# Optimization experiments

Hardware: AMD Instinct MI355X
Metric: run time of the kernel (lower is better)

The kernel has to match this reference:

```python
import jax, jax.numpy as jnp
import numpy as np

B, S, D, H = 2, 2048, 1024, 16
DH = D // H  # dim_per_head = 64


def setup_inputs() -> dict:
    key = jax.random.key(0)
    ks = jax.random.split(key, 12)
    scale = 1.0 / np.sqrt(D)
    inp = {
        "key": jax.random.normal(ks[0], (B, S, D), jnp.float32),
        "value": jax.random.normal(ks[1], (B, S, D), jnp.float32),
        "query": jax.random.normal(ks[2], (B, S, D), jnp.float32),
        "mask": jax.random.randint(ks[3], (B, S, S), 0, 2) == 1,
        "Wq": jax.random.normal(ks[4], (D, D), jnp.float32) * scale,
        "bq": jnp.zeros((D,), jnp.float32),
        "Wk": jax.random.normal(ks[5], (D, D), jnp.float32) * scale,
        "bk": jnp.zeros((D,), jnp.float32),
        "Wv": jax.random.normal(ks[6], (D, D), jnp.float32) * scale,
        "bv": jnp.zeros((D,), jnp.float32),
        "Wo": jax.random.normal(ks[7], (D, D), jnp.float32) * scale,
        "bo": jnp.zeros((D,), jnp.float32),
    }
    return inp


def reference(key, value, query, mask, Wq, bq, Wk, bk, Wv, bv, Wo, bo):
    b, s, d = query.shape
    dh = d // H

    def split_heads(x):  # [b, s, d] -> [b, H, s, dh]
        return x.reshape(b, -1, H, dh).transpose(0, 2, 1, 3)

    q = split_heads(query @ Wq + bq) / jnp.sqrt(jnp.float32(dh))
    k = split_heads(key @ Wk + bk)
    v = split_heads(value @ Wv + bv)

    scores = jnp.einsum("bhqd,bhkd->bhqk", q, k)  # [b, H, s, s]
    scores = jnp.where(mask[:, None, :, :], jnp.float32(-1e18), scores)
    attn = jax.nn.softmax(scores, axis=-1)  # dropout is identity in eval
    ctx = jnp.einsum("bhqk,bhkd->bhqd", attn, v)
    ctx = ctx.transpose(0, 2, 1, 3).reshape(b, s, d)
    return ctx @ Wo + bo
```

## Files before the change

kernel.cpp:

```cpp
#include <hip/hip_runtime.h>
#include <hip/hip_bf16.h>

#define BATCH  2
#define SEQ    2048
#define DMODEL 1024
#define NHEAD  16
#define DHEAD  64
#define NTOK   (BATCH * SEQ)

using f32x4 = __attribute__((ext_vector_type(4))) float;
using s16x4 = __attribute__((ext_vector_type(4))) short;
using s16x8 = __attribute__((ext_vector_type(8))) short;

__device__ __forceinline__ short f2bf(float f) {
  __hip_bfloat16 h = __float2bfloat16(f);
  return *(short*)&h;
}

__device__ __forceinline__ void gload_lds16(const short* g, short* l) {
  __builtin_amdgcn_global_load_lds(
      (const __attribute__((address_space(1))) void*)g,
      (__attribute__((address_space(3))) void*)l, 16, 0, 0);
}

__global__ __launch_bounds__(256) void wtrans_kernel(
    const float* __restrict__ Wq, const float* __restrict__ Wk,
    const float* __restrict__ Wv, const float* __restrict__ Wo,
    short* __restrict__ Wt) {
  __shared__ short tile[64][72];
  const float* W = blockIdx.z == 0 ? Wq : blockIdx.z == 1 ? Wk
                 : blockIdx.z == 2 ? Wv : Wo;
  short* out = Wt + (size_t)blockIdx.z * DMODEL * DMODEL;
  int k0 = blockIdx.x * 64, n0 = blockIdx.y * 64;
  int t = threadIdx.x;
#pragma unroll
  for (int i = 0; i < 4; ++i) {
    int idx = t + i * 256;
    int row = idx >> 4, c4 = idx & 15;
    f32x4 v = *(const f32x4*)(W + (size_t)(k0 + row) * DMODEL + n0 + c4 * 4);
    s16x4 p;
    p[0] = f2bf(v[0]); p[1] = f2bf(v[1]); p[2] = f2bf(v[2]); p[3] = f2bf(v[3]);
    *(s16x4*)&tile[row][c4 * 4] = p;
  }
  __syncthreads();
#pragma unroll
  for (int i = 0; i < 2; ++i) {
    int idx = t + i * 256;
    int nrow = idx >> 3, c8 = idx & 7;
    s16x8 p;
#pragma unroll
    for (int j = 0; j < 8; ++j) p[j] = tile[c8 * 8 + j][nrow];
    *(s16x8*)(out + (size_t)(n0 + nrow) * DMODEL + k0 + c8 * 8) = p;
  }
}

__global__ __launch_bounds__(256) void mpack_kernel(
    const int* __restrict__ mask, unsigned long long* __restrict__ Mp) {
  const int total_words = BATCH * SEQ * (SEQ / 64);
  int lane = threadIdx.x & 63;
  int wv = blockIdx.x * 4 + (threadIdx.x >> 6);
  int nw = gridDim.x * 4;
  for (int w = wv; w < total_words; w += nw) {
    int mv = mask[(size_t)w * 64 + lane];
    unsigned long long bits = __ballot(mv != 0);
    if (lane == 0) Mp[w] = bits;
  }
}

__global__ __launch_bounds__(256) void proj_qkv_kernel(
    const float* __restrict__ Xq, const float* __restrict__ Xk,
    const float* __restrict__ Xv, const short* __restrict__ Wt,
    const float* __restrict__ bq, const float* __restrict__ bk,
    const float* __restrict__ bv, short* __restrict__ QKV) {
  __shared__ short As[128][32];
  __shared__ short Bs[128][32];
  const int sel = blockIdx.z;
  const float* X    = sel == 0 ? Xq : sel == 1 ? Xk : Xv;
  const float* bias = sel == 0 ? bq : sel == 1 ? bk : bv;
  const short* Wsel = Wt + (size_t)sel * DMODEL * DMODEL;
  short* Obuf = QKV + (size_t)sel * ((size_t)BATCH * NHEAD * SEQ * DHEAD);
  const float scale = sel == 0 ? 0.18033688011111793f : 1.0f;

  int m0 = blockIdx.x * 128, n0 = blockIdx.y * 128;
  int t = threadIdx.x, wid = t >> 6, lane = t & 63;
  int lr = lane & 15, lg = lane >> 4;
  int wr = wid >> 1, wc = wid & 1;
  f32x4 acc[4][4] = {};

  for (int kt = 0; kt < DMODEL / 32; ++kt) {
    int k0 = kt * 32;
    __syncthreads();
#pragma unroll
    for (int i = 0; i < 2; ++i) {
      int c = i * 256 + t;
      short* lbase = &Bs[0][0] + (size_t)((i * 256 + (t & ~63)) << 3);
      gload_lds16(Wsel + (size_t)(n0 + (c >> 2)) * DMODEL + k0 + ((c & 3) << 3),
                  lbase);
    }
#pragma unroll
    for (int i = 0; i < 2; ++i) {
      int idx = t + i * 256, row = idx >> 2, c8 = idx & 3;
      const float* src = X + (size_t)(m0 + row) * DMODEL + k0 + c8 * 8;
      f32x4 v0 = *(const f32x4*)src;
      f32x4 v1 = *(const f32x4*)(src + 4);
      s16x8 p;
      p[0] = f2bf(v0[0]); p[1] = f2bf(v0[1]); p[2] = f2bf(v0[2]); p[3] = f2bf(v0[3]);
      p[4] = f2bf(v1[0]); p[5] = f2bf(v1[1]); p[6] = f2bf(v1[2]); p[7] = f2bf(v1[3]);
      *(s16x8*)&As[row][c8 * 8] = p;
    }
    __syncthreads();
    s16x8 afr[4], bfr[4];
#pragma unroll
    for (int mi = 0; mi < 4; ++mi)
      afr[mi] = *(const s16x8*)&As[wr * 64 + mi * 16 + lr][lg * 8];
#pragma unroll
    for (int ni = 0; ni < 4; ++ni)
      bfr[ni] = *(const s16x8*)&Bs[wc * 64 + ni * 16 + lr][lg * 8];
#pragma unroll
    for (int mi = 0; mi < 4; ++mi)
#pragma unroll
      for (int ni = 0; ni < 4; ++ni)
        acc[mi][ni] = __builtin_amdgcn_mfma_f32_16x16x32_bf16(
            afr[mi], bfr[ni], acc[mi][ni], 0, 0, 0);
  }
#pragma unroll
  for (int mi = 0; mi < 4; ++mi)
#pragma unroll
    for (int ni = 0; ni < 4; ++ni) {
      int n = n0 + wc * 64 + ni * 16 + lr;
      float bv_ = bias[n];
      int h = n >> 6, d = n & 63;
#pragma unroll
      for (int r = 0; r < 4; ++r) {
        int m = m0 + wr * 64 + mi * 16 + lg * 4 + r;
        int b = m >> 11, s = m & (SEQ - 1);
        float val = (acc[mi][ni][r] + bv_) * scale;
        Obuf[((size_t)(b * NHEAD + h) * SEQ + s) * DHEAD + d] = f2bf(val);
      }
    }
}

__global__ __launch_bounds__(256) void attn_kernel(
    const short* __restrict__ Qb, const short* __restrict__ Kb,
    const short* __restrict__ Vb, const unsigned long long* __restrict__ Mp,
    short* __restrict__ Ctx) {
  __shared__ short Ks[64][72];
  __shared__ short Vt[64][72];
  __shared__ short Ps[4][16][72];
  int qt = blockIdx.x, bh = blockIdx.y;
  int b = bh >> 4, h = bh & 15;
  int q0 = qt * 64;
  int t = threadIdx.x, wid = t >> 6, lane = t & 63;
  int lr = lane & 15, lg = lane >> 4;

  const short* Qrow = Qb + ((size_t)bh * SEQ + q0 + wid * 16 + lr) * DHEAD;
  s16x8 qf[2];
  qf[0] = *(const s16x8*)(Qrow + lg * 8);
  qf[1] = *(const s16x8*)(Qrow + 32 + lg * 8);

  float m_run = -1e30f, l_run = 0.f;
  f32x4 o_acc[4] = {};

  const unsigned long long* mrow =
      Mp + ((size_t)b * SEQ + q0 + wid * 16 + lr) * (SEQ / 64);

  for (int kt = 0; kt < SEQ / 64; ++kt) {
    int k0 = kt * 64;
    unsigned long long mw = mrow[kt];
    __syncthreads();
#pragma unroll
    for (int i = 0; i < 2; ++i) {
      int idx = t + i * 256, key = idx >> 3, c8 = idx & 7;
      *(s16x8*)&Ks[key][c8 * 8] =
          *(const s16x8*)(Kb + ((size_t)bh * SEQ + k0 + key) * DHEAD + c8 * 8);
    }
#pragma unroll
    for (int i = 0; i < 2; ++i) {
      int idx = t + i * 256, key = idx & 63, c8 = idx >> 6;
      s16x8 v = *(const s16x8*)(Vb + ((size_t)bh * SEQ + k0 + key) * DHEAD + c8 * 8);
#pragma unroll
      for (int j = 0; j < 8; ++j) Vt[c8 * 8 + j][key] = v[j];
    }
    __syncthreads();

    f32x4 sfr[4];
#pragma unroll
    for (int nf = 0; nf < 4; ++nf) {
      s16x8 kf0 = *(const s16x8*)&Ks[nf * 16 + lr][lg * 8];
      s16x8 kf1 = *(const s16x8*)&Ks[nf * 16 + lr][32 + lg * 8];
      f32x4 c = {};
      c = __builtin_amdgcn_mfma_f32_16x16x32_bf16(kf0, qf[0], c, 0, 0, 0);
      c = __builtin_amdgcn_mfma_f32_16x16x32_bf16(kf1, qf[1], c, 0, 0, 0);
      sfr[nf] = c;
    }
    unsigned w0 = (unsigned)(mw >> (lg * 4));
    unsigned w1 = (unsigned)(mw >> (lg * 4 + 32));
#pragma unroll
    for (int nf = 0; nf < 4; ++nf)
#pragma unroll
      for (int r = 0; r < 4; ++r) {
        unsigned bit = (nf < 2) ? (w0 >> (nf * 16 + r)) : (w1 >> ((nf - 2) * 16 + r));
        if (bit & 1u) sfr[nf][r] = -1e30f;
      }
    float tm = fmaxf(fmaxf(fmaxf(sfr[0][0], sfr[0][1]), fmaxf(sfr[0][2], sfr[0][3])),
                     fmaxf(fmaxf(sfr[1][0], sfr[1][1]), fmaxf(sfr[1][2], sfr[1][3])));
    float tm2 = fmaxf(fmaxf(fmaxf(sfr[2][0], sfr[2][1]), fmaxf(sfr[2][2], sfr[2][3])),
                      fmaxf(fmaxf(sfr[3][0], sfr[3][1]), fmaxf(sfr[3][2], sfr[3][3])));
    tm = fmaxf(tm, tm2);
    tm = fmaxf(tm, __shfl_xor(tm, 16, 64));
    tm = fmaxf(tm, __shfl_xor(tm, 32, 64));

    bool small = __all(tm <= m_run + 8.0f);
    if (!small) {
      float mnew = fmaxf(m_run, tm);
      float scl = __builtin_amdgcn_exp2f(m_run - mnew);
      m_run = mnew;
      l_run *= scl;
      float scl_o[4];
#pragma unroll
      for (int r = 0; r < 4; ++r) scl_o[r] = __shfl(scl, lg * 4 + r, 64);
#pragma unroll
      for (int nf = 0; nf < 4; ++nf)
#pragma unroll
        for (int r = 0; r < 4; ++r) o_acc[nf][r] *= scl_o[r];
    }
    float ps4[4];
#pragma unroll
    for (int nf = 0; nf < 4; ++nf) {
#pragma unroll
      for (int r = 0; r < 4; ++r)
        sfr[nf][r] = __builtin_amdgcn_exp2f(sfr[nf][r] - m_run);
      ps4[nf] = (sfr[nf][0] + sfr[nf][1]) + (sfr[nf][2] + sfr[nf][3]);
    }
    float ps = (ps4[0] + ps4[1]) + (ps4[2] + ps4[3]);
    ps += __shfl_xor(ps, 16, 64);
    ps += __shfl_xor(ps, 32, 64);
    l_run += ps;

#pragma unroll
    for (int nf = 0; nf < 4; ++nf) {
      s16x4 pk;
#pragma unroll
      for (int r = 0; r < 4; ++r) pk[r] = f2bf(sfr[nf][r]);
      *(s16x4*)&Ps[wid][lr][nf * 16 + lg * 4] = pk;
    }
    asm volatile("s_waitcnt lgkmcnt(0)" ::: "memory");
    __builtin_amdgcn_sched_barrier(0);

#pragma unroll
    for (int ks = 0; ks < 2; ++ks) {
      s16x8 pf = *(const s16x8*)&Ps[wid][lr][ks * 32 + lg * 8];
#pragma unroll
      for (int nf = 0; nf < 4; ++nf) {
        s16x8 vf = *(const s16x8*)&Vt[nf * 16 + lr][ks * 32 + lg * 8];
        o_acc[nf] = __builtin_amdgcn_mfma_f32_16x16x32_bf16(pf, vf, o_acc[nf], 0, 0, 0);
      }
    }
  }
  float l_o[4];
#pragma unroll
  for (int r = 0; r < 4; ++r) l_o[r] = __shfl(l_run, lg * 4 + r, 64);
#pragma unroll
  for (int nf = 0; nf < 4; ++nf)
#pragma unroll
    for (int r = 0; r < 4; ++r) {
      int srow = q0 + wid * 16 + lg * 4 + r;
      float val = o_acc[nf][r] / l_o[r];
      Ctx[((size_t)b * SEQ + srow) * DMODEL + h * DHEAD + nf * 16 + lr] = f2bf(val);
    }
}

__global__ __launch_bounds__(256) void proj_out_kernel(
    const short* __restrict__ Ctx, const short* __restrict__ Wot,
    const float* __restrict__ bo, float* __restrict__ Out) {
  __shared__ short As[128][32];
  __shared__ short Bs[128][32];
  int m0 = blockIdx.x * 128, n0 = blockIdx.y * 128;
  int t = threadIdx.x, wid = t >> 6, lane = t & 63;
  int lr = lane & 15, lg = lane >> 4;
  int wr = wid >> 1, wc = wid & 1;
  f32x4 acc[4][4] = {};

  for (int kt = 0; kt < DMODEL / 32; ++kt) {
    int k0 = kt * 32;
    __syncthreads();
#pragma unroll
    for (int i = 0; i < 2; ++i) {
      int c = i * 256 + t;
      size_t lofs = (size_t)((i * 256 + (t & ~63)) << 3);
      gload_lds16(Ctx + (size_t)(m0 + (c >> 2)) * DMODEL + k0 + ((c & 3) << 3),
                  &As[0][0] + lofs);
      gload_lds16(Wot + (size_t)(n0 + (c >> 2)) * DMODEL + k0 + ((c & 3) << 3),
                  &Bs[0][0] + lofs);
    }
    __syncthreads();
    s16x8 afr[4], bfr[4];
#pragma unroll
    for (int mi = 0; mi < 4; ++mi)
      afr[mi] = *(const s16x8*)&As[wr * 64 + mi * 16 + lr][lg * 8];
#pragma unroll
    for (int ni = 0; ni < 4; ++ni)
      bfr[ni] = *(const s16x8*)&Bs[wc * 64 + ni * 16 + lr][lg * 8];
#pragma unroll
    for (int mi = 0; mi < 4; ++mi)
#pragma unroll
      for (int ni = 0; ni < 4; ++ni)
        acc[mi][ni] = __builtin_amdgcn_mfma_f32_16x16x32_bf16(
            afr[mi], bfr[ni], acc[mi][ni], 0, 0, 0);
  }
#pragma unroll
  for (int mi = 0; mi < 4; ++mi)
#pragma unroll
    for (int ni = 0; ni < 4; ++ni) {
      int n = n0 + wc * 64 + ni * 16 + lr;
      float bv_ = bo[n];
#pragma unroll
      for (int r = 0; r < 4; ++r) {
        int m = m0 + wr * 64 + mi * 16 + lg * 4 + r;
        Out[(size_t)m * DMODEL + n] = acc[mi][ni][r] + bv_;
      }
    }
}

extern "C" void kernel_launch(void* const* d_in, const int* in_sizes, int n_in,
                              void* d_out, int out_size, void* d_ws, size_t ws_size,
                              hipStream_t stream) {
  const float* key_in   = (const float*)d_in[0];
  const float* value_in = (const float*)d_in[1];
  const float* query_in = (const float*)d_in[2];
  const int*   mask     = (const int*)d_in[3];
  const float* Wq = (const float*)d_in[4];
  const float* bq = (const float*)d_in[5];
  const float* Wk = (const float*)d_in[6];
  const float* bk = (const float*)d_in[7];
  const float* Wv = (const float*)d_in[8];
  const float* bv = (const float*)d_in[9];
  const float* Wo = (const float*)d_in[10];
  const float* bo = (const float*)d_in[11];
  float* out = (float*)d_out;

  short* ws = (short*)d_ws;
  const size_t WSZ   = (size_t)DMODEL * DMODEL;
  const size_t QKVSZ = (size_t)BATCH * NHEAD * SEQ * DHEAD;
  short* Wt  = ws;
  short* QKV = ws + 4 * WSZ;
  short* Qb  = QKV;
  short* Kb  = QKV + QKVSZ;
  short* Vb  = QKV + 2 * QKVSZ;
  short* Ctx = QKV + 3 * QKVSZ;
  unsigned long long* Mp = (unsigned long long*)ws;

  wtrans_kernel<<<dim3(16, 16, 4), 256, 0, stream>>>(Wq, Wk, Wv, Wo, Wt);
  proj_qkv_kernel<<<dim3(32, 8, 3), 256, 0, stream>>>(
      query_in, key_in, value_in, Wt, bq, bk, bv, QKV);
  mpack_kernel<<<dim3(1024), 256, 0, stream>>>(mask, Mp);
  attn_kernel<<<dim3(32, 32), 256, 0, stream>>>(Qb, Kb, Vb, Mp, Ctx);
  proj_out_kernel<<<dim3(32, 8), 256, 0, stream>>>(Ctx, Wt + 3 * WSZ, bo, out);
}
```

Baseline: 194.9 us.

## Prefetch next K/V tile into registers, XOR-swizzle LDS, and raise MFMA priority

The attention kernel now loads the next K/V tile and mask word into registers while the current tile is being computed, which hides global-load latency behind the MFMA work. The padded LDS arrays are replaced by unpadded ones with an XOR swizzle on 8-element chunks, so K, V-transpose and P accesses avoid bank conflicts with less shared memory. s_setprio is raised around the MFMA sections. The cost is extra registers for the prefetch buffers, which may reduce occupancy.

```diff
diff --git a/kernel.cpp b/kernel.cpp
--- a/kernel.cpp
+++ b/kernel.cpp
@@ -144,57 +144,79 @@
     const short* __restrict__ Qb, const short* __restrict__ Kb,
     const short* __restrict__ Vb, const unsigned long long* __restrict__ Mp,
     short* __restrict__ Ctx) {
-  __shared__ short Ks[64][72];
-  __shared__ short Vt[64][72];
-  __shared__ short Ps[4][16][72];
+  __shared__ short Ks[64 * 64];
+  __shared__ short Vt[64 * 64];
+  __shared__ short Ps[4 * 16 * 64];
   int qt = blockIdx.x, bh = blockIdx.y;
   int b = bh >> 4, h = bh & 15;
   int q0 = qt * 64;
   int t = threadIdx.x, wid = t >> 6, lane = t & 63;
   int lr = lane & 15, lg = lane >> 4;
+  int lr7 = lr & 7;
 
   const short* Qrow = Qb + ((size_t)bh * SEQ + q0 + wid * 16 + lr) * DHEAD;
   s16x8 qf[2];
   qf[0] = *(const s16x8*)(Qrow + lg * 8);
   qf[1] = *(const s16x8*)(Qrow + 32 + lg * 8);
 
+  const short* KbBase = Kb + (size_t)bh * SEQ * DHEAD;
+  const short* VbBase = Vb + (size_t)bh * SEQ * DHEAD;
+
   float m_run = -1e30f, l_run = 0.f;
   f32x4 o_acc[4] = {};
 
   const unsigned long long* mrow =
       Mp + ((size_t)b * SEQ + q0 + wid * 16 + lr) * (SEQ / 64);
+  unsigned long long mw = mrow[0];
+
+  s16x8 kreg[2], vreg[2];
+#pragma unroll
+  for (int i = 0; i < 2; ++i) {
+    kreg[i] = *(const s16x8*)(KbBase + (size_t)((t >> 3) + i * 32) * DHEAD + (t & 7) * 8);
+    vreg[i] = *(const s16x8*)(VbBase + (size_t)lane * DHEAD + (wid + i * 4) * 8);
+  }
 
   for (int kt = 0; kt < SEQ / 64; ++kt) {
-    int k0 = kt * 64;
-    unsigned long long mw = mrow[kt];
+    unsigned long long mw_cur = mw;
     __syncthreads();
 #pragma unroll
     for (int i = 0; i < 2; ++i) {
-      int idx = t + i * 256, key = idx >> 3, c8 = idx & 7;
-      *(s16x8*)&Ks[key][c8 * 8] =
-          *(const s16x8*)(Kb + ((size_t)bh * SEQ + k0 + key) * DHEAD + c8 * 8);
-    }
-#pragma unroll
-    for (int i = 0; i < 2; ++i) {
-      int idx = t + i * 256, key = idx & 63, c8 = idx >> 6;
-      s16x8 v = *(const s16x8*)(Vb + ((size_t)bh * SEQ + k0 + key) * DHEAD + c8 * 8);
-#pragma unroll
-      for (int j = 0; j < 8; ++j) Vt[c8 * 8 + j][key] = v[j];
-    }
-    __syncthreads();
+      int krow = (t >> 3) + i * 32, kc = t & 7;
+      *(s16x8*)&Ks[krow * 64 + ((kc ^ (krow & 7)) << 3)] = kreg[i];
+      int vc8 = wid + i * 4;
+#pragma unroll
+      for (int j = 0; j < 8; ++j) {
+        int d = vc8 * 8 + j;
+        Vt[d * 64 + ((((lane >> 3) ^ (d & 7)) << 3) | (lane & 7))] = vreg[i][j];
+      }
+    }
+    __syncthreads();
+    if (kt + 1 < SEQ / 64) {
+      int k0n = (kt + 1) * 64;
+#pragma unroll
+      for (int i = 0; i < 2; ++i) {
+        kreg[i] = *(const s16x8*)(KbBase + (size_t)(k0n + (t >> 3) + i * 32) * DHEAD + (t & 7) * 8);
+        vreg[i] = *(const s16x8*)(VbBase + (size_t)(k0n + lane) * DHEAD + (wid + i * 4) * 8);
+      }
+      mw = mrow[kt + 1];
+    }
 
     f32x4 sfr[4];
+    __builtin_amdgcn_s_setprio(1);
 #pragma unroll
     for (int nf = 0; nf < 4; ++nf) {
-      s16x8 kf0 = *(const s16x8*)&Ks[nf * 16 + lr][lg * 8];
-      s16x8 kf1 = *(const s16x8*)&Ks[nf * 16 + lr][32 + lg * 8];
+      int row = nf * 16 + lr;
+      s16x8 kf0 = *(const s16x8*)&Ks[row * 64 + ((lg ^ lr7) << 3)];
+      s16x8 kf1 = *(const s16x8*)&Ks[row * 64 + (((4 + lg) ^ lr7) << 3)];
       f32x4 c = {};
       c = __builtin_amdgcn_mfma_f32_16x16x32_bf16(kf0, qf[0], c, 0, 0, 0);
       c = __builtin_amdgcn_mfma_f32_16x16x32_bf16(kf1, qf[1], c, 0, 0, 0);
       sfr[nf] = c;
     }
-    unsigned w0 = (unsigned)(mw >> (lg * 4));
-    unsigned w1 = (unsigned)(mw >> (lg * 4 + 32));
+    __builtin_amdgcn_s_setprio(0);
+
+    unsigned w0 = (unsigned)(mw_cur >> (lg * 4));
+    unsigned w1 = (unsigned)(mw_cur >> (lg * 4 + 32));
 #pragma unroll
     for (int nf = 0; nf < 4; ++nf)
 #pragma unroll
@@ -237,25 +259,29 @@
     ps += __shfl_xor(ps, 32, 64);
     l_run += ps;
 
+    int psbase = wid * (16 * 64) + lr * 64;
 #pragma unroll
     for (int nf = 0; nf < 4; ++nf) {
       s16x4 pk;
 #pragma unroll
       for (int r = 0; r < 4; ++r) pk[r] = f2bf(sfr[nf][r]);
-      *(s16x4*)&Ps[wid][lr][nf * 16 + lg * 4] = pk;
+      *(s16x4*)&Ps[psbase + ((((2 * nf + (lg >> 1)) ^ lr7) << 3) | ((lg & 1) << 2))] = pk;
     }
     asm volatile("s_waitcnt lgkmcnt(0)" ::: "memory");
     __builtin_amdgcn_sched_barrier(0);
 
+    __builtin_amdgcn_s_setprio(1);
 #pragma unroll
     for (int ks = 0; ks < 2; ++ks) {
-      s16x8 pf = *(const s16x8*)&Ps[wid][lr][ks * 32 + lg * 8];
+      s16x8 pf = *(const s16x8*)&Ps[psbase + (((ks * 4 + lg) ^ lr7) << 3)];
 #pragma unroll
       for (int nf = 0; nf < 4; ++nf) {
-        s16x8 vf = *(const s16x8*)&Vt[nf * 16 + lr][ks * 32 + lg * 8];
+        int d = nf * 16 + lr;
+        s16x8 vf = *(const s16x8*)&Vt[d * 64 + (((ks * 4 + lg) ^ lr7) << 3)];
         o_acc[nf] = __builtin_amdgcn_mfma_f32_16x16x32_bf16(pf, vf, o_acc[nf], 0, 0, 0);
       }
     }
+    __builtin_amdgcn_s_setprio(0);
   }
   float l_o[4];
 #pragma unroll
```

Measured after the change: 195.7 us. About the same (+0.4%).
